# Optimization experiments

Hardware: AMD Instinct MI355X
Metric: run time of the kernel (lower is better)

The kernel has to match this reference:

```python
import jax, jax.numpy as jnp
import numpy as np
from jax import lax

TAU = 0.25
N_TIMESTEPS = 12
OUTPUT_TICKS = 4
INPUT_DIM = 1024
HIDDEN = 1024
OUTPUT_DIM = 1024
CLEANUP = 512
BATCH = 1024
W_SD = 0.1


def setup_inputs() -> dict:
    key = jax.random.key(0)
    ks = jax.random.split(key, 6)
    inputs = jax.random.normal(ks[0], (BATCH, N_TIMESTEPS, INPUT_DIM), dtype=jnp.float32)
    w_oh = W_SD * jax.random.normal(ks[1], (INPUT_DIM, HIDDEN), dtype=jnp.float32)
    w_hp = W_SD * jax.random.normal(ks[2], (HIDDEN, OUTPUT_DIM), dtype=jnp.float32)
    w_pp = W_SD * jax.random.normal(ks[3], (OUTPUT_DIM, OUTPUT_DIM), dtype=jnp.float32)
    w_pc = W_SD * jax.random.normal(ks[4], (OUTPUT_DIM, CLEANUP), dtype=jnp.float32)
    w_cp = W_SD * jax.random.normal(ks[5], (CLEANUP, OUTPUT_DIM), dtype=jnp.float32)
    bias_h = jnp.zeros((HIDDEN,), jnp.float32)
    bias_p = jnp.zeros((OUTPUT_DIM,), jnp.float32)
    bias_c = jnp.zeros((CLEANUP,), jnp.float32)
    return {"inputs": inputs, "w_oh": w_oh, "w_hp": w_hp, "w_pp": w_pp,
            "w_pc": w_pc, "w_cp": w_cp, "bias_h": bias_h, "bias_p": bias_p,
            "bias_c": bias_c}


def reference(inputs, w_oh, w_hp, w_pp, w_pc, w_cp, bias_h, bias_p, bias_c):
    B = inputs.shape[0]
    act = jax.nn.sigmoid
    # time-major input stream: step t consumes o_input[:, t-1, :]
    x = jnp.swapaxes(inputs, 0, 1)  # [T, B, I]

    in_h0 = jnp.zeros((B, HIDDEN), jnp.float32)
    in_p0 = jnp.zeros((B, OUTPUT_DIM), jnp.float32)
    in_c0 = jnp.zeros((B, CLEANUP), jnp.float32)
    carry0 = (in_h0, in_p0, in_c0, in_h0 + 0.5, in_p0 + 0.5, in_c0 + 0.5)

    def step(carry, o_t):
        in_h, in_p, in_c, a_h, a_p, a_c = carry
        # leaky-integrator blends; hp/pp/cp/pc all use PREVIOUS step activations
        h = TAU * (o_t @ w_oh + bias_h) + (1.0 - TAU) * in_h
        p = TAU * (a_h @ w_hp + a_p @ w_pp + a_c @ w_cp + bias_p) + (1.0 - TAU) * in_p
        c = TAU * (a_p @ w_pc + bias_c) + (1.0 - TAU) * in_c
        a_p_new = act(p)
        new_carry = (h, p, c, act(h), a_p_new, act(c))
        return new_carry, a_p_new

    _, act_p_seq = lax.scan(step, carry0, x)  # [T, B, OUTPUT_DIM]
    return act_p_seq[-OUTPUT_TICKS:]  # [OUTPUT_TICKS, B, OUTPUT_DIM]
```

## Files before the change

### kernel.cpp

```cpp
#include <hip/hip_runtime.h>
#include <cstdint>
#include <cstddef>


typedef _Float16 half8 __attribute__((ext_vector_type(8)));
typedef float floatx4 __attribute__((ext_vector_type(4)));

__device__ __forceinline__ void async_cp16(const void* g, void* l) {
  __builtin_amdgcn_global_load_lds(
      (const __attribute__((address_space(1))) void*)g,
      (__attribute__((address_space(3))) void*)l, 16, 0, 0);
}

__device__ __forceinline__ float sigmoidf_(float x) {
  return 1.f / (1.f + __expf(-x));
}

__global__ __launch_bounds__(256) void k_transpose(
    const float* __restrict__ src, int K, int N,
    _Float16* __restrict__ dst, int dst_ld, int k_off) {
  __shared__ float tile[64][65];
  const int k0 = blockIdx.y * 64, n0 = blockIdx.x * 64;
  const int tx = threadIdx.x & 63, ty = threadIdx.x >> 6;
#pragma unroll
  for (int j = 0; j < 16; ++j) {
    int kr = j * 4 + ty;
    tile[kr][tx] = src[(size_t)(k0 + kr) * N + n0 + tx];
  }
  __syncthreads();
#pragma unroll
  for (int j = 0; j < 16; ++j) {
    int nr = j * 4 + ty;
    dst[(size_t)(n0 + nr) * dst_ld + k_off + k0 + tx] = (_Float16)tile[tx][nr];
  }
}

__global__ __launch_bounds__(256) void k_pack_frag(
    const float* __restrict__ src, int N, _Float16* __restrict__ dst,
    int kStride, int kOffChunks) {
  __shared__ float tile[64][65];
  const int k0 = blockIdx.y * 64, n0 = blockIdx.x * 64;
  const int tx = threadIdx.x & 63, ty = threadIdx.x >> 6;
#pragma unroll
  for (int jj = 0; jj < 16; ++jj) {
    int kr = jj * 4 + ty;
    tile[kr][tx] = src[(size_t)(k0 + kr) * N + n0 + tx];
  }
  __syncthreads();
  const int j = threadIdx.x >> 6, lane = threadIdx.x & 63;
  const int r16 = lane & 15, quad = lane >> 4;
#pragma unroll
  for (int c = 0; c < 2; ++c) {
    half8 v;
#pragma unroll
    for (int u = 0; u < 8; ++u)
      v[u] = (_Float16)tile[c * 32 + quad * 8 + u][j * 16 + r16];
    const int kcG = kOffChunks + blockIdx.y * 2 + c;
    *(half8*)(dst + ((size_t)(blockIdx.x * kStride + kcG) * 4 + j) * 512 +
              lane * 8) = v;
  }
}

__global__ __launch_bounds__(256) void k_prep(
    const float* __restrict__ x, _Float16* __restrict__ U,
    _Float16* __restrict__ AH0, _Float16* __restrict__ AP0,
    _Float16* __restrict__ AC0, float* __restrict__ Pst,
    float* __restrict__ Cst) {
  const int id = blockIdx.x * 256 + threadIdx.x;
  const int b = id >> 10, i = id & 1023;
  const float* xb = x + (size_t)b * 12 * 1024 + i;
  float g = 0.f;
#pragma unroll
  for (int t = 0; t < 11; ++t) {
    g = xb[t * 1024] + 0.75f * g;
    U[(size_t)t * 1048576 + id] = (_Float16)g;
  }
  AH0[id] = (_Float16)0.5f;
  AP0[id] = (_Float16)0.5f;
  Pst[id] = 0.f;
  if (i < 512) {
    const int cid = b * 512 + i;
    AC0[cid] = (_Float16)0.5f;
    Cst[cid] = 0.f;
  }
}

__global__ __launch_bounds__(256, 3) void k_gemm_big(
    const _Float16* __restrict__ A, const _Float16* __restrict__ B,
    const float* __restrict__ bias, _Float16* __restrict__ dst, int mode) {
  __shared__ __align__(16) _Float16 sA[128 * 64];
  __shared__ __align__(16) _Float16 sB[128 * 64];
  const int tid = threadIdx.x;
  const int lane = tid & 63, w = tid >> 6;
  const int mBase = blockIdx.y * 128, nBase = blockIdx.x * 128;
  const int r16 = lane & 15, quad = lane >> 4;
  const int lrow = lane >> 3;
  const int gsw = ((lane & 7) ^ lrow) * 8;
  const int wr = w >> 1, wc = w & 1;

  const floatx4 zero = {0.f, 0.f, 0.f, 0.f};
  floatx4 acc[4][4];
#pragma unroll
  for (int i = 0; i < 4; ++i)
#pragma unroll
    for (int j = 0; j < 4; ++j) acc[i][j] = zero;

  const _Float16* Abase = A + (size_t)(mBase + w * 32 + lrow) * 1024 + gsw;
  const _Float16* Bbase = B + (size_t)(nBase + w * 32 + lrow) * 1024 + gsw;
  _Float16* sAw = sA + (w * 32) * 64;
  _Float16* sBw = sB + (w * 32) * 64;
  const _Float16* sa = sA + (size_t)wr * 64 * 64;
  const _Float16* sb = sB + (size_t)wc * 64 * 64;

  for (int kt = 0; kt < 16; ++kt) {
    const int k0 = kt << 6;
#pragma unroll
    for (int q = 0; q < 4; ++q)
      async_cp16(Abase + (size_t)q * 8192 + k0, sAw + q * 512);
#pragma unroll
    for (int q = 0; q < 4; ++q)
      async_cp16(Bbase + (size_t)q * 8192 + k0, sBw + q * 512);
    asm volatile("s_waitcnt vmcnt(0)" ::: "memory");
    __syncthreads();
#pragma unroll
    for (int kk = 0; kk < 2; ++kk) {
      const int sw = ((kk * 4 + quad) ^ (r16 & 7)) * 8;
      half8 af[4], bf[4];
#pragma unroll
      for (int i = 0; i < 4; ++i)
        af[i] = *(const half8*)&sa[(i * 16 + r16) * 64 + sw];
#pragma unroll
      for (int j = 0; j < 4; ++j)
        bf[j] = *(const half8*)&sb[(j * 16 + r16) * 64 + sw];
#pragma unroll
      for (int i = 0; i < 4; ++i)
#pragma unroll
        for (int j = 0; j < 4; ++j)
          acc[i][j] = __builtin_amdgcn_mfma_f32_16x16x32_f16(af[i], bf[j],
                                                             acc[i][j], 0, 0, 0);
    }
    __syncthreads();
  }

  if (mode == 0) {
    const int tm1 = mBase >> 10;
    const float beta = 1.f - __powf(0.75f, (float)(tm1 + 1));
    _Float16* o = dst + (size_t)(mBase + 1024) * 1024;
#pragma unroll
    for (int i = 0; i < 4; ++i)
#pragma unroll
      for (int j = 0; j < 4; ++j) {
        const int n = nBase + wc * 64 + j * 16 + r16;
#pragma unroll
        for (int r = 0; r < 4; ++r) {
          const int row = wr * 64 + i * 16 + quad * 4 + r;
          const float h = 0.25f * acc[i][j][r] + beta * bias[n];
          o[(size_t)row * 1024 + n] = (_Float16)sigmoidf_(h);
        }
      }
  } else {
    _Float16* o = dst + (size_t)mBase * 1024;
#pragma unroll
    for (int i = 0; i < 4; ++i)
#pragma unroll
      for (int j = 0; j < 4; ++j) {
        const int n = nBase + wc * 64 + j * 16 + r16;
#pragma unroll
        for (int r = 0; r < 4; ++r) {
          const int row = wr * 64 + i * 16 + quad * 4 + r;
          o[(size_t)row * 1024 + n] = (_Float16)(0.25f * (acc[i][j][r] + bias[n]));
        }
      }
  }
}

__global__ __launch_bounds__(256, 3) void k_step(
    const _Float16* __restrict__ Qt, const _Float16* __restrict__ APc,
    const _Float16* __restrict__ ACc, _Float16* __restrict__ APn,
    _Float16* __restrict__ ACn, const _Float16* __restrict__ Wrf,
    const _Float16* __restrict__ Wcf, const float* __restrict__ bias_c,
    float* __restrict__ Pst, float* __restrict__ Cst,
    float* __restrict__ out_t) {
  __shared__ float red[4][2][4][4][64];
  const int lane = threadIdx.x & 63, w = threadIdx.x >> 6;
  const int r16 = lane & 15, quad = lane >> 4;
  const int blk = blockIdx.x;
  const bool isP = blk < 512;
  int mBase, nt;
  if (isP) {
    mBase = (blk >> 4) * 32;
    nt = blk & 15;
  } else {
    const int b = blk - 512;
    mBase = (b >> 3) * 32;
    nt = b & 7;
  }
  const int nBase = nt * 64;
  const floatx4 zero = {0.f, 0.f, 0.f, 0.f};
  floatx4 acc[2][4];
#pragma unroll
  for (int i = 0; i < 2; ++i)
#pragma unroll
    for (int j = 0; j < 4; ++j) acc[i][j] = zero;

  half8 abuf[3][2], bbuf[3][4];
  auto MM = [&](half8* af, half8* bf) {
#pragma unroll
    for (int i = 0; i < 2; ++i)
#pragma unroll
      for (int j = 0; j < 4; ++j)
        acc[i][j] = __builtin_amdgcn_mfma_f32_16x16x32_f16(af[i], bf[j],
                                                           acc[i][j], 0, 0, 0);
  };

  if (isP) {
    const int kcBase = w * 12;
    auto LD = [&](half8* af, half8* bf, int c) {
      const int kc = kcBase + c;
      const int kg = kc * 32;
      if (kc < 32) {
#pragma unroll
        for (int i = 0; i < 2; ++i)
          af[i] = *(const half8*)(APc + (size_t)(mBase + i * 16 + r16) * 1024 +
                                  kg + quad * 8);
      } else {
#pragma unroll
        for (int i = 0; i < 2; ++i)
          af[i] = *(const half8*)(ACc + (size_t)(mBase + i * 16 + r16) * 512 +
                                  (kg - 1024) + quad * 8);
      }
      const _Float16* wp = Wrf + (size_t)(nt * 48 + kc) * 2048 + lane * 8;
#pragma unroll
      for (int j = 0; j < 4; ++j) bf[j] = *(const half8*)(wp + j * 512);
    };
    LD(abuf[0], bbuf[0], 0);
    LD(abuf[1], bbuf[1], 1);
#pragma unroll
    for (int c = 0; c < 12; ++c) {
      if (c + 2 < 12) LD(abuf[(c + 2) % 3], bbuf[(c + 2) % 3], c + 2);
      MM(abuf[c % 3], bbuf[c % 3]);
    }
  } else {
    const int kcBase = w * 8;
    auto LD = [&](half8* af, half8* bf, int c) {
      const int kc = kcBase + c;
      const int kg = kc * 32;
#pragma unroll
      for (int i = 0; i < 2; ++i)
        af[i] = *(const half8*)(APc + (size_t)(mBase + i * 16 + r16) * 1024 +
                                kg + quad * 8);
      const _Float16* wp = Wcf + (size_t)(nt * 32 + kc) * 2048 + lane * 8;
#pragma unroll
      for (int j = 0; j < 4; ++j) bf[j] = *(const half8*)(wp + j * 512);
    };
    LD(abuf[0], bbuf[0], 0);
    LD(abuf[1], bbuf[1], 1);
#pragma unroll
    for (int c = 0; c < 8; ++c) {
      if (c + 2 < 8) LD(abuf[(c + 2) % 3], bbuf[(c + 2) % 3], c + 2);
      MM(abuf[c % 3], bbuf[c % 3]);
    }
  }

#pragma unroll
  for (int i = 0; i < 2; ++i)
#pragma unroll
    for (int j = 0; j < 4; ++j)
#pragma unroll
      for (int r = 0; r < 4; ++r) red[w][i][j][r][lane] = acc[i][j][r];
  __syncthreads();

  if (isP) {
#pragma unroll
    for (int i = 0; i < 2; ++i) {
      const int n = nBase + w * 16 + r16;
#pragma unroll
      for (int r = 0; r < 4; ++r) {
        const float v = red[0][i][w][r][lane] + red[1][i][w][r][lane] +
                        red[2][i][w][r][lane] + red[3][i][w][r][lane];
        const int b = mBase + i * 16 + quad * 4 + r;
        const size_t o = (size_t)b * 1024 + n;
        const float pn = 0.25f * v + (float)Qt[o] + 0.75f * Pst[o];
        Pst[o] = pn;
        const float a = sigmoidf_(pn);
        APn[o] = (_Float16)a;
        if (out_t) out_t[o] = a;
      }
    }
  } else {
#pragma unroll
    for (int i = 0; i < 2; ++i) {
      const int n = nBase + w * 16 + r16;
#pragma unroll
      for (int r = 0; r < 4; ++r) {
        const float v = red[0][i][w][r][lane] + red[1][i][w][r][lane] +
                        red[2][i][w][r][lane] + red[3][i][w][r][lane];
        const int b = mBase + i * 16 + quad * 4 + r;
        const size_t o = (size_t)b * 512 + n;
        const float cn = 0.25f * (v + bias_c[n]) + 0.75f * Cst[o];
        Cst[o] = cn;
        ACn[o] = (_Float16)sigmoidf_(cn);
      }
    }
  }
}

extern "C" void kernel_launch(void* const* d_in, const int* in_sizes, int n_in,
                              void* d_out, int out_size, void* d_ws,
                              size_t ws_size, hipStream_t stream) {
  const float* x      = (const float*)d_in[0];
  const float* w_oh   = (const float*)d_in[1];
  const float* w_hp   = (const float*)d_in[2];
  const float* w_pp   = (const float*)d_in[3];
  const float* w_pc   = (const float*)d_in[4];
  const float* w_cp   = (const float*)d_in[5];
  const float* bias_h = (const float*)d_in[6];
  const float* bias_p = (const float*)d_in[7];
  const float* bias_c = (const float*)d_in[8];
  float* out = (float*)d_out;

  uint8_t* p = (uint8_t*)d_ws;
  _Float16* Wrf  = (_Float16*)p; p += (size_t)1024 * 1536 * 2;
  _Float16* Wcf  = (_Float16*)p; p += (size_t)512 * 1024 * 2;
  _Float16* WohT = (_Float16*)p; p += (size_t)1024 * 1024 * 2;
  _Float16* Whp  = (_Float16*)p; p += (size_t)1024 * 1024 * 2;
  _Float16* U    = (_Float16*)p; p += (size_t)11 * 1048576 * 2;
  _Float16* AH   = (_Float16*)p; p += (size_t)12 * 1048576 * 2;
  _Float16* Q    = (_Float16*)p; p += (size_t)12 * 1048576 * 2;
  _Float16* AP0  = (_Float16*)p; p += (size_t)1048576 * 2;
  _Float16* AP1  = (_Float16*)p; p += (size_t)1048576 * 2;
  _Float16* AC0  = (_Float16*)p; p += (size_t)512 * 1024 * 2;
  _Float16* AC1  = (_Float16*)p; p += (size_t)512 * 1024 * 2;
  float* Pst = (float*)p; p += (size_t)1048576 * 4;
  float* Cst = (float*)p; p += (size_t)512 * 1024 * 4;

  const dim3 blk256(256);
  k_transpose<<<dim3(16, 16), blk256, 0, stream>>>(w_oh, 1024, 1024, WohT, 1024, 0);
  k_transpose<<<dim3(16, 16), blk256, 0, stream>>>(w_hp, 1024, 1024, Whp, 1024, 0);
  k_pack_frag<<<dim3(16, 16), blk256, 0, stream>>>(w_pp, 1024, Wrf, 48, 0);
  k_pack_frag<<<dim3(16, 8),  blk256, 0, stream>>>(w_cp, 1024, Wrf, 48, 32);
  k_pack_frag<<<dim3(8, 16),  blk256, 0, stream>>>(w_pc, 512, Wcf, 32, 0);
  k_prep<<<4096, blk256, 0, stream>>>(x, U, AH, AP0, AC0, Pst, Cst);
  k_gemm_big<<<dim3(8, 88), blk256, 0, stream>>>(U, WohT, bias_h, AH, 0);
  k_gemm_big<<<dim3(8, 96), blk256, 0, stream>>>(AH, Whp, bias_p, Q, 1);
  for (int t = 0; t < 12; ++t) {
    const _Float16* APc = (t & 1) ? AP1 : AP0;
    _Float16* APn       = (t & 1) ? AP0 : AP1;
    const _Float16* ACc = (t & 1) ? AC1 : AC0;
    _Float16* ACn       = (t & 1) ? AC0 : AC1;
    float* ot = (t >= 8) ? out + (size_t)(t - 8) * 1048576 : (float*)nullptr;
    k_step<<<dim3(768), blk256, 0, stream>>>(Q + (size_t)t * 1048576, APc,
                                             ACc, APn, ACn, Wrf, Wcf, bias_c,
                                             Pst, Cst, ot);
  }
}
```

Baseline: 395.0 us.

## Stream weight tiles into LDS ring via async loads and prefetch epilogue operands

The recurrent-step kernel now copies weight fragments with global_load_lds into a per-wave three-slot LDS ring, gated by explicit vmcnt waits. Activation fragments are still loaded into registers but prefetched four chunks ahead. Epilogue state reads (Qt, Pst, Cst, bias) are issued before the reduction barrier so their latency overlaps it. The goal is deeper overlap of memory latency with MFMA work, at the cost of 48KB of LDS per block, which may lower occupancy. Hand-computed waitcnt values are fragile if the compiler reorders memory operations.

Result: slower. 419.1 us (+6.1%).

```diff
diff --git a/kernel.cpp b/kernel.cpp
--- a/kernel.cpp
+++ b/kernel.cpp
@@ -174,6 +174,26 @@
   }
 }
 
+#define KCHUNK(c, NC)                                                         \
+  {                                                                           \
+    if ((c) + 2 < (NC)) LDB((c) + 2);                                         \
+    asm volatile("s_waitcnt vmcnt(%0)" ::"i"(                                 \
+        2 * ((((c) + 2 >= 4 && (c) + 2 < (NC)) ? 1 : 0) +                     \
+             (((c) + 3 >= 4 && (c) + 3 < (NC)) ? 1 : 0)) +                    \
+        4 * ((((c) + 1 < (NC)) ? 1 : 0) + (((c) + 2 < (NC)) ? 1 : 0)))        \
+                 : "memory");                                                 \
+    {                                                                         \
+      const _Float16* sp_ = ringw + ((c) % 3) * 2048 + lane * 8;              \
+      half8 bf_[4];                                                           \
+      bf_[0] = *(const half8*)(sp_);                                          \
+      bf_[1] = *(const half8*)(sp_ + 512);                                    \
+      bf_[2] = *(const half8*)(sp_ + 1024);                                   \
+      bf_[3] = *(const half8*)(sp_ + 1536);                                   \
+      MM(abuf[(c) & 3], bf_);                                                 \
+    }                                                                         \
+    if ((c) + 4 < (NC)) LDA((c) + 4);                                         \
+  }
+
 __global__ __launch_bounds__(256, 3) void k_step(
     const _Float16* __restrict__ Qt, const _Float16* __restrict__ APc,
     const _Float16* __restrict__ ACc, _Float16* __restrict__ APn,
@@ -181,9 +201,12 @@
     const _Float16* __restrict__ Wcf, const float* __restrict__ bias_c,
     float* __restrict__ Pst, float* __restrict__ Cst,
     float* __restrict__ out_t) {
-  __shared__ float red[4][2][4][4][64];
+  __shared__ __align__(16) unsigned char smraw[49152];
   const int lane = threadIdx.x & 63, w = threadIdx.x >> 6;
   const int r16 = lane & 15, quad = lane >> 4;
+  _Float16* ringw = (_Float16*)(smraw + w * 12288);
+  float* red = (float*)smraw;
+
   const int blk = blockIdx.x;
   const bool isP = blk < 512;
   int mBase, nt;
@@ -203,7 +226,7 @@
 #pragma unroll
     for (int j = 0; j < 4; ++j) acc[i][j] = zero;
 
-  half8 abuf[3][2], bbuf[3][4];
+  half8 abuf[4][2];
   auto MM = [&](half8* af, half8* bf) {
 #pragma unroll
     for (int i = 0; i < 2; ++i)
@@ -215,72 +238,103 @@
 
   if (isP) {
     const int kcBase = w * 12;
-    auto LD = [&](half8* af, half8* bf, int c) {
+    auto LDA = [&](int c) {
+      const int kc = kcBase + c, kg = kc * 32;
+      half8* af = abuf[c & 3];
+      if (kc < 32) {
+        af[0] = *(const half8*)(APc + (size_t)(mBase + r16) * 1024 + kg + quad * 8);
+        af[1] = *(const half8*)(APc + (size_t)(mBase + 16 + r16) * 1024 + kg + quad * 8);
+      } else {
+        af[0] = *(const half8*)(ACc + (size_t)(mBase + r16) * 512 + (kg - 1024) + quad * 8);
+        af[1] = *(const half8*)(ACc + (size_t)(mBase + 16 + r16) * 512 + (kg - 1024) + quad * 8);
+      }
+    };
+    auto LDB = [&](int c) {
       const int kc = kcBase + c;
-      const int kg = kc * 32;
-      if (kc < 32) {
-#pragma unroll
-        for (int i = 0; i < 2; ++i)
-          af[i] = *(const half8*)(APc + (size_t)(mBase + i * 16 + r16) * 1024 +
-                                  kg + quad * 8);
-      } else {
-#pragma unroll
-        for (int i = 0; i < 2; ++i)
-          af[i] = *(const half8*)(ACc + (size_t)(mBase + i * 16 + r16) * 512 +
-                                  (kg - 1024) + quad * 8);
-      }
       const _Float16* wp = Wrf + (size_t)(nt * 48 + kc) * 2048 + lane * 8;
-#pragma unroll
-      for (int j = 0; j < 4; ++j) bf[j] = *(const half8*)(wp + j * 512);
+      _Float16* d = ringw + (c % 3) * 2048;
+      async_cp16(wp, d);
+      async_cp16(wp + 512, d + 512);
+      async_cp16(wp + 1024, d + 1024);
+      async_cp16(wp + 1536, d + 1536);
     };
-    LD(abuf[0], bbuf[0], 0);
-    LD(abuf[1], bbuf[1], 1);
-#pragma unroll
-    for (int c = 0; c < 12; ++c) {
-      if (c + 2 < 12) LD(abuf[(c + 2) % 3], bbuf[(c + 2) % 3], c + 2);
-      MM(abuf[c % 3], bbuf[c % 3]);
-    }
+    LDA(0); LDA(1); LDA(2); LDA(3);
+    LDB(0); LDB(1);
+    KCHUNK(0, 12) KCHUNK(1, 12) KCHUNK(2, 12) KCHUNK(3, 12)
+    KCHUNK(4, 12) KCHUNK(5, 12) KCHUNK(6, 12) KCHUNK(7, 12)
+    KCHUNK(8, 12) KCHUNK(9, 12) KCHUNK(10, 12) KCHUNK(11, 12)
   } else {
     const int kcBase = w * 8;
-    auto LD = [&](half8* af, half8* bf, int c) {
+    auto LDA = [&](int c) {
+      const int kc = kcBase + c, kg = kc * 32;
+      half8* af = abuf[c & 3];
+      af[0] = *(const half8*)(APc + (size_t)(mBase + r16) * 1024 + kg + quad * 8);
+      af[1] = *(const half8*)(APc + (size_t)(mBase + 16 + r16) * 1024 + kg + quad * 8);
+    };
+    auto LDB = [&](int c) {
       const int kc = kcBase + c;
-      const int kg = kc * 32;
-#pragma unroll
-      for (int i = 0; i < 2; ++i)
-        af[i] = *(const half8*)(APc + (size_t)(mBase + i * 16 + r16) * 1024 +
-                                kg + quad * 8);
       const _Float16* wp = Wcf + (size_t)(nt * 32 + kc) * 2048 + lane * 8;
-#pragma unroll
-      for (int j = 0; j < 4; ++j) bf[j] = *(const half8*)(wp + j * 512);
+      _Float16* d = ringw + (c % 3) * 2048;
+      async_cp16(wp, d);
+      async_cp16(wp + 512, d + 512);
+      async_cp16(wp + 1024, d + 1024);
+      async_cp16(wp + 1536, d + 1536);
     };
-    LD(abuf[0], bbuf[0], 0);
-    LD(abuf[1], bbuf[1], 1);
-#pragma unroll
-    for (int c = 0; c < 8; ++c) {
-      if (c + 2 < 8) LD(abuf[(c + 2) % 3], bbuf[(c + 2) % 3], c + 2);
-      MM(abuf[c % 3], bbuf[c % 3]);
-    }
-  }
-
+    LDA(0); LDA(1); LDA(2); LDA(3);
+    LDB(0); LDB(1);
+    KCHUNK(0, 8) KCHUNK(1, 8) KCHUNK(2, 8) KCHUNK(3, 8)
+    KCHUNK(4, 8) KCHUNK(5, 8) KCHUNK(6, 8) KCHUNK(7, 8)
+  }
+
+  const int n_ep = nBase + w * 16 + r16;
+  _Float16 qv[2][4];
+  float pv[2][4];
+  float cv[2][4];
+  float biasn = 0.f;
+  if (isP) {
+#pragma unroll
+    for (int i = 0; i < 2; ++i)
+#pragma unroll
+      for (int r = 0; r < 4; ++r) {
+        const size_t o = (size_t)(mBase + i * 16 + quad * 4 + r) * 1024 + n_ep;
+        qv[i][r] = Qt[o];
+        pv[i][r] = Pst[o];
+      }
+  } else {
+    biasn = bias_c[n_ep];
+#pragma unroll
+    for (int i = 0; i < 2; ++i)
+#pragma unroll
+      for (int r = 0; r < 4; ++r) {
+        const size_t o = (size_t)(mBase + i * 16 + quad * 4 + r) * 512 + n_ep;
+        cv[i][r] = Cst[o];
+      }
+  }
+
+  asm volatile("s_waitcnt lgkmcnt(0)" ::: "memory");
+  __builtin_amdgcn_s_barrier();
 #pragma unroll
   for (int i = 0; i < 2; ++i)
 #pragma unroll
     for (int j = 0; j < 4; ++j)
 #pragma unroll
-      for (int r = 0; r < 4; ++r) red[w][i][j][r][lane] = acc[i][j][r];
-  __syncthreads();
+      for (int r = 0; r < 4; ++r)
+        red[((((w * 2 + i) * 4 + j) * 4 + r) * 64) + lane] = acc[i][j][r];
+  asm volatile("s_waitcnt lgkmcnt(0)" ::: "memory");
+  __builtin_amdgcn_s_barrier();
 
   if (isP) {
 #pragma unroll
     for (int i = 0; i < 2; ++i) {
-      const int n = nBase + w * 16 + r16;
 #pragma unroll
       for (int r = 0; r < 4; ++r) {
-        const float v = red[0][i][w][r][lane] + red[1][i][w][r][lane] +
-                        red[2][i][w][r][lane] + red[3][i][w][r][lane];
+        float v = 0.f;
+#pragma unroll
+        for (int q = 0; q < 4; ++q)
+          v += red[((((q * 2 + i) * 4 + w) * 4 + r) * 64) + lane];
         const int b = mBase + i * 16 + quad * 4 + r;
-        const size_t o = (size_t)b * 1024 + n;
-        const float pn = 0.25f * v + (float)Qt[o] + 0.75f * Pst[o];
+        const size_t o = (size_t)b * 1024 + n_ep;
+        const float pn = 0.25f * v + (float)qv[i][r] + 0.75f * pv[i][r];
         Pst[o] = pn;
         const float a = sigmoidf_(pn);
         APn[o] = (_Float16)a;
@@ -290,14 +344,15 @@
   } else {
 #pragma unroll
     for (int i = 0; i < 2; ++i) {
-      const int n = nBase + w * 16 + r16;
 #pragma unroll
       for (int r = 0; r < 4; ++r) {
-        const float v = red[0][i][w][r][lane] + red[1][i][w][r][lane] +
-                        red[2][i][w][r][lane] + red[3][i][w][r][lane];
+        float v = 0.f;
+#pragma unroll
+        for (int q = 0; q < 4; ++q)
+          v += red[((((q * 2 + i) * 4 + w) * 4 + r) * 64) + lane];
         const int b = mBase + i * 16 + quad * 4 + r;
-        const size_t o = (size_t)b * 512 + n;
-        const float cn = 0.25f * (v + bias_c[n]) + 0.75f * Cst[o];
+        const size_t o = (size_t)b * 512 + n_ep;
+        const float cn = 0.25f * (v + biasn) + 0.75f * cv[i][r];
         Cst[o] = cn;
         ACn[o] = (_Float16)sigmoidf_(cn);
       }
```
